# Kernel tuning notes

Measured on AMD Instinct MI355X. Metric: run time of the kernel, lower is better.

Reference implementation:

```python
import jax, jax.numpy as jnp
import numpy as np
from jax import lax

NUM_SUPERNODES = 1024
KNN_K = 16
MIN_GRIPPER = 16
MIN_MASK = 8
GRIP_START = 0
GRIP_RADIUS = 0.1
NEG_INF = -jnp.inf


def _take(a, idx):
    return jnp.take_along_axis(a, idx, axis=1)


def _scatter_or(idx, keep, Bf, N):
    # OR `keep` into a fresh [Bf,N] bool mask at positions idx (mirrors torch scatter_)
    b = jnp.arange(Bf)[:, None]
    return jnp.zeros((Bf, N), dtype=bool).at[b, idx].max(keep)


def _cdist(a, b):
    # a [B,M,3], b [B,N,3] -> [B,M,N] euclidean
    d2 = (jnp.sum(a * a, -1)[:, :, None] + jnp.sum(b * b, -1)[:, None, :]
          - 2.0 * jnp.einsum('bmd,bnd->bmn', a, b))
    return jnp.sqrt(jnp.maximum(d2, 0.0))


def _sample_supernodes(xyz, valid, state, mask_id, extra_scores, global_scores):
    Bf, N, _ = xyz.shape
    M = NUM_SUPERNODES
    valid = valid.astype(bool)
    row_has_valid = valid.any(axis=1)
    first_valid = jnp.argmax(valid, axis=1).astype(jnp.int32)  # [Bf]

    # ---- gripper quota: nearest points to gripper xyz (within radius if any) ----
    k_grip = min(MIN_GRIPPER, M)
    gxyz = state[:, GRIP_START:GRIP_START + 3]
    gdist = jnp.linalg.norm(xyz - gxyz[:, None, :], axis=-1)  # [Bf,N]
    in_radius = gdist <= GRIP_RADIUS
    has_radius = (valid & in_radius).any(axis=1, keepdims=True)
    eligible = valid & (in_radius | ~has_radius)
    dist_rank = jnp.where(eligible, gdist, jnp.inf)
    neg_vals, grip_idx = lax.top_k(-dist_rank, k_grip)
    grip_vals = -neg_vals
    grip_keep = jnp.isfinite(grip_vals) & row_has_valid[:, None]
    head_idx = jnp.where(grip_keep, grip_idx, first_valid[:, None])
    head_bucket = jnp.where(grip_keep, 1, -1)
    selected = _scatter_or(grip_idx, grip_keep, Bf, N)

    remaining = M - k_grip
    # ---- mask-instance quota: one point per mask id (dedup via sort) ----
    mask_cand = valid & ~selected
    sentinel = jnp.iinfo(mask_id.dtype).max
    mask_key = jnp.where(mask_cand, mask_id, sentinel)
    sort_idx = jnp.argsort(mask_key, axis=1)
    sorted_valid = _take(mask_cand, sort_idx)
    sorted_mask = _take(mask_id, sort_idx)
    first_for_id = jnp.concatenate(
        [sorted_valid[:, :1],
         sorted_valid[:, 1:] & (sorted_mask[:, 1:] != sorted_mask[:, :-1])], axis=1)
    pos = jnp.arange(N, dtype=jnp.float32)[None, :]
    mask_scores = jnp.where(first_for_id, -pos, NEG_INF)
    mask_vals, mask_pos = lax.top_k(mask_scores, remaining)
    mask_idx = _take(sort_idx, mask_pos)
    mask_keep = jnp.isfinite(mask_vals) & row_has_valid[:, None]
    selected_after_mask = selected | _scatter_or(mask_idx, mask_keep, Bf, N)

    # ---- extra random mask supernodes to guarantee min_mask quota ----
    k_extra = min(MIN_MASK, remaining)
    es = jnp.where(valid & ~selected_after_mask, extra_scores, NEG_INF)
    extra_vals, extra_idx = lax.top_k(es, k_extra)
    extra_keep = jnp.isfinite(extra_vals) & row_has_valid[:, None]
    use_extra = ~mask_keep[:, :k_extra] & extra_keep
    mask_idx = mask_idx.at[:, :k_extra].set(
        jnp.where(use_extra, extra_idx, mask_idx[:, :k_extra]))
    mask_keep = mask_keep.at[:, :k_extra].set(mask_keep[:, :k_extra] | use_extra)

    # ---- global random fill ----
    selected_for_global = selected | _scatter_or(mask_idx, mask_keep, Bf, N)
    gs = jnp.where(valid & ~selected_for_global, global_scores, NEG_INF)
    gvals, gidx = lax.top_k(gs, remaining)
    gkeep = jnp.isfinite(gvals) & row_has_valid[:, None]
    fill_idx = jnp.where(mask_keep, mask_idx,
                         jnp.where(gkeep, gidx, first_valid[:, None]))
    fill_bucket = jnp.where(mask_keep, 2, jnp.where(gkeep, 0, -1))

    out_idx = jnp.concatenate([head_idx, fill_idx], axis=1)
    out_bucket = jnp.concatenate([head_bucket, fill_bucket], axis=1)
    out_valid = _take(valid, out_idx) & row_has_valid[:, None]
    out_bucket = jnp.where(out_valid, out_bucket, -1)
    return out_idx, out_valid, out_bucket


def setup_inputs() -> dict:
    key = jax.random.key(0)
    ks = jax.random.split(key, 6)
    Bf, N, C = 8, 16384, 64
    return {
        'x': jax.random.normal(ks[0], (Bf, N, C), dtype=jnp.float32),
        'xyz': jax.random.normal(ks[1], (Bf, N, 3), dtype=jnp.float32),
        'valid': jnp.ones((Bf, N), dtype=bool),
        'state': jax.random.normal(ks[2], (Bf, 8), dtype=jnp.float32),
        'mask_id': jax.random.randint(ks[3], (Bf, N), 0, 32, dtype=jnp.int32),
        'extra_scores': jax.random.uniform(ks[4], (Bf, N), dtype=jnp.float32),
        'global_scores': jax.random.uniform(ks[5], (Bf, N), dtype=jnp.float32),
    }


def reference(x, xyz, valid, state, mask_id, extra_scores, global_scores):
    Bf, N, C = x.shape
    out_idx, out_valid, out_bucket = _sample_supernodes(
        xyz, valid, state, mask_id, extra_scores, global_scores)
    # gather_points
    supernode_xyz = _take(xyz, out_idx[:, :, None].repeat(3, axis=2))  # [Bf,M,3]
    # build_knn_neighbors: masked cdist + topk smallest
    dist = _cdist(supernode_xyz.astype(jnp.float32), xyz.astype(jnp.float32))
    dist = jnp.where(valid.astype(bool)[:, None, :], dist, jnp.inf)
    neg_vals, neighbor_idx = lax.top_k(-dist, KNN_K)
    neighbor_mask = jnp.isfinite(-neg_vals)  # [Bf,M,K]
    # gather_neighbors
    b = jnp.arange(Bf)[:, None, None]
    neighbor_feats = x[b, neighbor_idx]  # [Bf,M,K,C]
    return (neighbor_feats, supernode_xyz, neighbor_mask,
            out_idx, out_valid, out_bucket)
```

## Files before the change

### kernel.cpp

```cpp
#include <hip/hip_runtime.h>
#include <math.h>

typedef unsigned long long u64;
typedef unsigned int u32;

#define BF 8
#define NPTS 16384
#define HALFPTS 8192
#define M_SN 1024
#define CCH 64
#define KNN 16
#define NTHR1 1024
#define KPER 16
#define TBL 4096
#define CCAP 2048
#define REM 1008

constexpr size_t O0 = 0;
constexpr size_t O1 = 8388608;
constexpr size_t O2 = 8413184;
constexpr size_t O3 = 8544256;
constexpr size_t O4 = 8552448;
constexpr size_t O5 = 8560640;

#define PW_OFF ((size_t)256)
#define PW_BYTES ((size_t)BF * NPTS * 16)
#define WN_BYTES ((size_t)2 * BF * M_SN * KNN * 8)

__device__ __forceinline__ bool is_valid_el(const void* vp, int mode, long long i) {
  if (mode == 1) return ((const unsigned char*)vp)[i] != 0;
  if (mode == 2) return ((const float*)vp)[i] != 0.0f;
  return ((const int*)vp)[i] != 0;
}

__device__ __forceinline__ u32 desc_enc(float f) {
  u32 u = __float_as_uint(f);
  u32 s = (u & 0x80000000u) ? ~u : (u | 0x80000000u);
  return ~s;
}
__device__ __forceinline__ float desc_dec(u32 e) {
  u32 s = ~e;
  u32 u = (s & 0x80000000u) ? (s & 0x7FFFFFFFu) : ~s;
  return __uint_as_float(u);
}
__device__ __forceinline__ bool enc_finite(u32 d) {
  u32 s = ~d;
  u32 u = (s & 0x80000000u) ? (s & 0x7FFFFFFFu) : ~s;
  return (u & 0x7F800000u) != 0x7F800000u;
}

__device__ __forceinline__ u64 wave_min_u64(u64 v) {
#pragma unroll
  for (int d = 32; d >= 1; d >>= 1) {
    u32 lo = __shfl_xor((u32)(v & 0xFFFFFFFFu), d, 64);
    u32 hi = __shfl_xor((u32)(v >> 32), d, 64);
    u64 o = ((u64)hi << 32) | lo;
    if (o < v) v = o;
  }
  return v;
}

__device__ __forceinline__ u64 block_min_u64(u64 v, u64* red16, int t) {
  v = wave_min_u64(v);
  if ((t & 63) == 0) red16[t >> 6] = v;
  __syncthreads();
  if (t < 64) {
    u64 x = red16[t & 15];
    x = wave_min_u64(x);
    if (t == 0) red16[0] = x;
  }
  __syncthreads();
  u64 r = red16[0];
  __syncthreads();
  return r;
}

__device__ __forceinline__ int block_excl_scan(int val, int* scanb, int t, int* tot) {
  int incl = val;
#pragma unroll
  for (int d = 1; d < 64; d <<= 1) {
    int v = __shfl_up(incl, d, 64);
    if ((t & 63) >= d) incl += v;
  }
  if ((t & 63) == 63) scanb[t >> 6] = incl;
  __syncthreads();
  if (t < 64) {
    int ws = (t < 16) ? scanb[t] : 0;
#pragma unroll
    for (int d = 1; d < 16; d <<= 1) {
      int v = __shfl_up(ws, d, 64);
      if ((t & 63) >= d) ws += v;
    }
    if (t < 16) scanb[16 + t] = ws;
  }
  __syncthreads();
  int wv = t >> 6;
  int base = (wv == 0) ? 0 : scanb[16 + wv - 1];
  *tot = scanb[16 + 15];
  int r = base + incl - val;
  __syncthreads();
  return r;
}

__device__ __forceinline__ u64 shfl64_grp(u64 v, int src) {
  u32 lo = (u32)__shfl((int)(u32)(v & 0xFFFFFFFFu), src, 32);
  u32 hi = (u32)__shfl((int)(u32)(v >> 32), src, 32);
  return ((u64)hi << 32) | lo;
}

template<bool ASC, bool SHIFTBIN>
__device__ __forceinline__ void topk_select(const u32* ek, const u32* bk, u32 cmask,
    int Twant, int* table, u64* cand, int* scanb, int* sh, int* outArr, int t) {
  for (int j = t; j < TBL; j += NTHR1) table[j] = 0;
  if (t == 6) sh[6] = 0x7FFFFFFF;
  if (t == 7) sh[7] = 1;
  __syncthreads();
#pragma unroll
  for (int k = 0; k < KPER; k++) {
    if ((cmask >> k) & 1u) {
      int bin = SHIFTBIN ? (int)(ek[k] >> 20) : (int)bk[k];
      atomicAdd(&table[bin], 1);
    }
  }
  __syncthreads();
  int c_[4]; int c4 = 0;
#pragma unroll
  for (int q = 0; q < 4; q++) { c_[q] = table[4 * t + q]; c4 += c_[q]; }
  int htot;
  int cum = block_excl_scan(c4, scanb, t, &htot);
  const int T = min(Twant, htot);
  int e_ = cum;
#pragma unroll
  for (int q = 0; q < 4; q++) {
    int nx = e_ + c_[q];
    if (T > 0 && e_ < T && nx >= T) atomicMin(&sh[6], 4 * t + q);
    table[4 * t + q] = e_;
    e_ = nx;
  }
  __syncthreads();
  if (T <= 0) return;
  const int B = sh[6];
#pragma unroll
  for (int k = 0; k < KPER; k++) {
    if ((cmask >> k) & 1u) {
      int bin = SHIFTBIN ? (int)(ek[k] >> 20) : (int)bk[k];
      if (bin <= B) {
        int pos = atomicAdd(&table[bin], 1);
        if (pos < CCAP)
          cand[pos] = ((u64)ek[k] << 32) | ((u64)(u32)bin << 14) | (u32)(k * NTHR1 + t);
      }
    }
  }
  __syncthreads();
  const int nc = table[B];
  if (nc <= CCAP) {
    for (int c = t; c < nc; c += NTHR1) {
      u64 key = cand[c];
      int bin = (int)((key >> 14) & 0xFFFu);
      int s = bin ? table[bin - 1] : 0;
      int e2 = table[bin];
      int r = s;
      for (int j = s; j < e2; j++) r += (cand[j] < key);
      if (r < T) {
        u32 enc = (u32)(key >> 32);
        int ix = (int)(key & 0x3FFFu);
        bool fin = ASC ? (enc < 0x7F800000u) : enc_finite(enc);
        outArr[r] = fin ? ix : (ix | (int)0x80000000);
      }
    }
  } else {
    if (t == 0) sh[7] = 0;
  }
  __syncthreads();
}

__global__ void detect_valid(const unsigned* __restrict__ w, int nwords, int* __restrict__ flag) {
  int local = 0;
  for (int i = blockIdx.x * blockDim.x + threadIdx.x; i < nwords; i += gridDim.x * blockDim.x) {
    unsigned v = w[i];
    if (v == 0x3F800000u) local = 2;
    else if (v != 0u && v != 1u) local = max(local, 1);
  }
#pragma unroll
  for (int d = 32; d >= 1; d >>= 1) local = max(local, __shfl_xor(local, d, 64));
  if ((threadIdx.x & 63) == 0 && local) atomicMax(flag, local);
}

__global__ __launch_bounds__(1024)
void sample_kernel(const float* __restrict__ xyz, const void* __restrict__ validp,
                   const float* __restrict__ state, const int* __restrict__ mask_id,
                   const float* __restrict__ extra, const float* __restrict__ glob,
                   const int* __restrict__ flagp, float4* __restrict__ pw,
                   float* __restrict__ out) {
  __shared__ u64 red16[16];
  __shared__ int table[TBL];
  __shared__ int scanb[32];
  __shared__ int mpick[REM];
  __shared__ u64 cand[CCAP];
  __shared__ int gsorted[REM];
  __shared__ int head_i[16];
  __shared__ int head_bk[16];
  __shared__ int sh[8];

  const int b = blockIdx.x, t = threadIdx.x;
  const int vmode = flagp[0];
  const float* xyzb = xyz + (size_t)b * NPTS * 3;
  const int* midb = mask_id + (size_t)b * NPTS;
  const float* exb = extra + (size_t)b * NPTS;
  const float* glb = glob + (size_t)b * NPTS;

  if (t < 8) sh[t] = 0;
  if (t == 1) sh[1] = 0x7FFFFFFF;
  if (t < 16) gsorted[t] = -1;
  __syncthreads();

  u32 vbits = 0;
#pragma unroll
  for (int k = 0; k < KPER; k++) {
    int i = k * NTHR1 + t;
    if (is_valid_el(validp, vmode, (long long)b * NPTS + i)) vbits |= 1u << k;
  }
  if (vbits) {
    atomicOr(&sh[0], 1);
    atomicMin(&sh[1], (__ffs(vbits) - 1) * NTHR1 + t);
  }

  float gx = state[b * 8 + 0], gy = state[b * 8 + 1], gz = state[b * 8 + 2];
  float gd[KPER];
  u32 inr = 0;
#pragma unroll
  for (int k = 0; k < KPER; k++) {
    int i = k * NTHR1 + t;
    float px = xyzb[3 * i], py = xyzb[3 * i + 1], pz = xyzb[3 * i + 2];
    float dx = px - gx, dy = py - gy, dz = pz - gz;
    float d = sqrtf((dx * dx + dy * dy) + dz * dz);
    gd[k] = d;
    bool vb = (vbits >> k) & 1u;
    if (vb && d <= 0.1f) inr |= 1u << k;
    if (pw) {
      float sb = __fadd_rn(__fadd_rn(__fmul_rn(px, px), __fmul_rn(py, py)), __fmul_rn(pz, pz));
      pw[(size_t)b * NPTS + i] = make_float4(px, py, pz, vb ? sb : INFINITY);
    }
  }
  if (inr) atomicOr(&sh[2], 1);
  __syncthreads();

  const int rhv = sh[0];
  const int first_valid = rhv ? sh[1] : 0;
  const u32 elig = vbits & (sh[2] ? inr : 0xFFFFu);
  u32 sel = 0;

  {
    u32 ek[KPER];
#pragma unroll
    for (int k = 0; k < KPER; k++) ek[k] = __float_as_uint(gd[k]);
    topk_select<true, true>(ek, nullptr, elig, 16, table, cand, scanb, sh, gsorted, t);
    if (sh[7]) {
      if (t < 16) {
        int g = gsorted[t];
        head_i[t] = (g >= 0) ? g : first_valid;
        head_bk[t] = (g >= 0) ? 1 : -1;
      }
      __syncthreads();
      for (int j = 0; j < 16; j++) {
        if (head_bk[j] == 1) {
          int ix = head_i[j];
          if ((ix & (NTHR1 - 1)) == t) sel |= 1u << (ix >> 10);
        }
      }
    } else {
      for (int it = 0; it < 16; ++it) {
        u64 best = ~0ull;
#pragma unroll
        for (int k = 0; k < KPER; k++) {
          if (((elig >> k) & 1u) && !((sel >> k) & 1u)) {
            u64 key = ((u64)__float_as_uint(gd[k]) << 32) | (u32)(k * NTHR1 + t);
            if (key < best) best = key;
          }
        }
        u64 w = block_min_u64(best, red16, t);
        bool keep = (w >> 32) < 0x7F800000ull;
        int idx = (int)(w & 0xFFFFFFFFu);
        if (t == 0) { head_i[it] = keep ? idx : first_valid; head_bk[it] = keep ? 1 : -1; }
        if (keep && (idx & (NTHR1 - 1)) == t) sel |= 1u << (idx >> 10);
      }
      __syncthreads();
    }
  }

  for (int j = t; j < TBL; j += NTHR1) table[j] = 0x7FFFFFFF;
  __syncthreads();
#pragma unroll
  for (int k = 0; k < KPER; k++) {
    if (((vbits >> k) & 1u) && !((sel >> k) & 1u)) {
      int i = k * NTHR1 + t;
      int id = midb[i];
      if ((u32)id < TBL) atomicMin(&table[id], i);
    }
  }
  __syncthreads();
  int cnt = 0;
#pragma unroll
  for (int q = 0; q < 4; q++) cnt += (table[4 * t + q] != 0x7FFFFFFF);
  int mtot;
  int excl = block_excl_scan(cnt, scanb, t, &mtot);
  {
    int pos = excl;
#pragma unroll
    for (int q = 0; q < 4; q++) {
      int v = table[4 * t + q];
      if (v != 0x7FFFFFFF) { if (pos < REM) mpick[pos] = v; pos++; }
    }
  }
  __syncthreads();
  const int nm = min(mtot, REM);
  for (int j = 0; j < nm; j++) {
    int p = mpick[j];
    if ((p & (NTHR1 - 1)) == t) sel |= 1u << (p >> 10);
  }

  u32 extra_used = 0;
  if (nm < 8 && rhv) {
    u32 extrbits = 0;
    for (int j = 0; j < 8; j++) {
      u64 best = ~0ull;
#pragma unroll
      for (int k = 0; k < KPER; k++) {
        if (((vbits >> k) & 1u) && !((sel >> k) & 1u) && !((extrbits >> k) & 1u)) {
          int i = k * NTHR1 + t;
          u64 key = ((u64)desc_enc(exb[i]) << 32) | (u32)i;
          if (key < best) best = key;
        }
      }
      u64 w = block_min_u64(best, red16, t);
      if (w == ~0ull) break;
      int idx = (int)(w & 0xFFFFFFFFu);
      bool fin = enc_finite((u32)(w >> 32));
      if ((idx & (NTHR1 - 1)) == t) extrbits |= 1u << (idx >> 10);
      if (j >= nm && fin) {
        extra_used |= 1u << j;
        if (t == 0) mpick[j] = idx;
        if ((idx & (NTHR1 - 1)) == t) sel |= 1u << (idx >> 10);
      }
    }
    __syncthreads();
  }

  {
    u32 cbits = vbits & ~sel;
    u32 ek[KPER], bk[KPER];
#pragma unroll
    for (int k = 0; k < KPER; k++) {
      if ((cbits >> k) & 1u) {
        float f = glb[k * NTHR1 + t];
        ek[k] = desc_enc(f);
        float g = fminf(fmaxf(f, 0.0f), 0.99999994f);
        bk[k] = 4095u - (u32)(g * 4096.0f);
      } else { ek[k] = 0xFFFFFFFFu; bk[k] = 4095u; }
    }
    for (int j = t; j < REM; j += NTHR1) gsorted[j] = -1;
    topk_select<false, false>(ek, bk, cbits, REM, table, cand, scanb, sh, gsorted, t);
    if (!sh[7]) {
      u32 gext = 0;
      for (int j = 0; j < REM; j++) {
        u64 best = ~0ull;
#pragma unroll
        for (int k = 0; k < KPER; k++) {
          if (((cbits >> k) & 1u) && !((gext >> k) & 1u)) {
            u64 key = ((u64)ek[k] << 32) | (u32)(k * NTHR1 + t);
            if (key < best) best = key;
          }
        }
        u64 w = block_min_u64(best, red16, t);
        if (w == ~0ull) break;
        int idx = (int)(w & 0xFFFFFFFFu);
        if ((idx & (NTHR1 - 1)) == t) gext |= 1u << (idx >> 10);
        if (t == 0) gsorted[j] = enc_finite((u32)(w >> 32)) ? idx : (idx | (int)0x80000000);
      }
      __syncthreads();
    }
  }

  {
    int slot = t;
    int idx, bucket;
    if (slot < 16) {
      idx = head_i[slot];
      bucket = head_bk[slot];
    } else {
      int jj = slot - 16;
      bool mk = (jj < nm) || (jj < 8 && ((extra_used >> jj) & 1u));
      if (mk) { idx = mpick[jj]; bucket = 2; }
      else {
        int g = gsorted[jj];
        if (rhv && g >= 0) { idx = g; bucket = 0; }
        else { idx = first_valid; bucket = -1; }
      }
    }
    bool ov = rhv && is_valid_el(validp, vmode, (long long)b * NPTS + idx);
    int ob = ov ? bucket : -1;
    size_t o = (size_t)b * M_SN + slot;
    out[O3 + o] = (float)idx;
    out[O4 + o] = ov ? 1.0f : 0.0f;
    out[O5 + o] = (float)ob;
    out[O1 + 3 * o + 0] = xyzb[3 * idx + 0];
    out[O1 + 3 * o + 1] = xyzb[3 * idx + 1];
    out[O1 + 3 * o + 2] = xyzb[3 * idx + 2];
  }
}

#define NTHR2 256
#define CH 1024
#define SPW 2
#define SNB 8
#define SPB 8

__global__ __launch_bounds__(256, 8)
void knn_kernel(const float* __restrict__ x, const float* __restrict__ xyz,
                const void* __restrict__ validp, const int* __restrict__ flagp,
                const float4* __restrict__ pw, u64* __restrict__ wnws,
                float* __restrict__ out) {
  __shared__ __align__(16) float4 st[CH];
  __shared__ u64 wn[SNB * KNN];

  const int b = blockIdx.x >> 7;
  const int grp = blockIdx.x & 127;
  const int half = blockIdx.y;
  const int t = threadIdx.x;
  const int g = t >> 6;
  const int lane = t & 63;
  const int m0 = grp * SNB + g * SPW;
  const float* xyzb = xyz + (size_t)b * NPTS * 3;
  const long long gbase = (long long)b * NPTS;

  float a2x[SPW], a2y[SPW], a2z[SPW];
#pragma unroll
  for (int s = 0; s < SPW; s++) {
    int sidx = (int)out[O3 + (size_t)b * M_SN + m0 + s];
    float ax, ay, az;
    if (pw) { float4 c = pw[gbase + sidx]; ax = c.x; ay = c.y; az = c.z; }
    else { ax = xyzb[3 * sidx]; ay = xyzb[3 * sidx + 1]; az = xyzb[3 * sidx + 2]; }
    a2x[s] = ax + ax; a2y[s] = ay + ay; a2z[s] = az + az;
  }

  float ld[SPW]; int li[SPW]; float kq[SPW];
#pragma unroll
  for (int s = 0; s < SPW; s++) { ld[s] = -INFINITY; li[s] = 0; kq[s] = -INFINITY; }

  const int vmode = pw ? 0 : flagp[0];
  const int cbeg = wnws ? half * HALFPTS : 0;
  const int cend = wnws ? cbeg + HALFPTS : NPTS;

  for (int c0 = cbeg; c0 < cend; c0 += CH) {
    if (pw) {
      const float4* src = pw + gbase + c0;
#pragma unroll
      for (int qq = 0; qq < CH / NTHR2; qq++) st[t + qq * NTHR2] = src[t + qq * NTHR2];
    } else {
      for (int p = t; p < CH; p += NTHR2) {
        float px = xyzb[3 * (c0 + p)], py = xyzb[3 * (c0 + p) + 1], pz = xyzb[3 * (c0 + p) + 2];
        bool v = is_valid_el(validp, vmode, gbase + c0 + p);
        float sb = __fadd_rn(__fadd_rn(__fmul_rn(px, px), __fmul_rn(py, py)), __fmul_rn(pz, pz));
        st[p] = make_float4(px, py, pz, v ? sb : INFINITY);
      }
    }
    __syncthreads();

    int jstart = 0;
    if (c0 == cbeg) {
      float4 v = st[lane];
#pragma unroll
      for (int s = 0; s < SPW; s++) {
        float qv = __builtin_fmaf(a2x[s], v.x, __builtin_fmaf(a2y[s], v.y, __builtin_fmaf(a2z[s], v.z, -v.w)));
        u64 ku = ((u64)desc_enc(qv) << 32) | (u32)(c0 + lane);
#pragma unroll
        for (int kk = 2; kk <= 64; kk <<= 1) {
#pragma unroll
          for (int jj = kk >> 1; jj > 0; jj >>= 1) {
            u32 olo = (u32)__shfl_xor((int)(u32)(ku & 0xFFFFFFFFu), jj, 64);
            u32 ohi = (u32)__shfl_xor((int)(u32)(ku >> 32), jj, 64);
            u64 o = ((u64)ohi << 32) | olo;
            bool keepmin = ((lane & jj) == 0) == ((lane & kk) == 0);
            ku = ((ku < o) == keepmin) ? ku : o;
          }
        }
        ld[s] = desc_dec((u32)(ku >> 32));
        li[s] = (int)(u32)(ku & 0xFFFFFFFFu);
        kq[s] = __shfl(ld[s], 15, 64);
      }
      jstart = 1;
    }

#pragma unroll 2
    for (int j = jstart; j < CH / 64; j++) {
      float4 v = st[lane + 64 * j];
#pragma unroll
      for (int s = 0; s < SPW; s++) {
        float qv = __builtin_fmaf(a2x[s], v.x, __builtin_fmaf(a2y[s], v.y, __builtin_fmaf(a2z[s], v.z, -v.w)));
        u64 bal = __ballot(qv > kq[s]);
        if (bal) {
          do {
            int bb = __ffsll(bal) - 1;
            bal &= bal - 1;
            float kd = __shfl(qv, bb, 64);
            int ki = c0 + 64 * j + bb;
            bool gt = ld[s] < kd;
            float sd = __shfl_up(ld[s], 1, 64);
            int si = __shfl_up(li[s], 1, 64);
            int pg = __shfl_up(gt ? 1 : 0, 1, 64);
            if (lane == 0) pg = 0;
            ld[s] = gt ? (pg ? sd : kd) : ld[s];
            li[s] = gt ? (pg ? si : ki) : li[s];
          } while (bal);
          kq[s] = __shfl(ld[s], 15, 64);
        }
      }
    }
    __syncthreads();
  }

  if (wnws) {
#pragma unroll
    for (int s = 0; s < SPW; s++)
      if (lane < KNN)
        wnws[((size_t)half * BF + b) * M_SN * KNN + (size_t)(m0 + s) * KNN + lane] =
            ((u64)desc_enc(ld[s]) << 32) | (u32)li[s];
    return;
  }

#pragma unroll
  for (int s = 0; s < SPW; s++)
    if (lane < KNN) wn[(g * SPW + s) * KNN + lane] = ((u64)desc_enc(ld[s]) << 32) | (u32)li[s];
  __syncthreads();
  for (int r = t; r < SNB * KNN; r += NTHR2) {
    u64 key = wn[r];
    int ni = (int)(key & (u64)(NPTS - 1));
    int mm = grp * SNB + (r >> 4);
    size_t o2 = ((size_t)b * M_SN + mm) * KNN + (r & 15);
    out[O2 + o2] = enc_finite((u32)(key >> 32)) ? 1.0f : 0.0f;
    const float4* src = (const float4*)(x + (gbase + ni) * CCH);
    float4* dst = (float4*)(out + O0 + o2 * CCH);
#pragma unroll
    for (int q = 0; q < 16; q++) dst[q] = src[q];
  }
}

__global__ __launch_bounds__(256)
void knn_merge_kernel(const float* __restrict__ x, const u64* __restrict__ wnws,
                      float* __restrict__ out) {
  __shared__ u64 wn[SPB * KNN];
  const int b = blockIdx.x >> 7;
  const int grp = blockIdx.x & 127;
  const int t = threadIdx.x;
  const int sl = t >> 5;
  const int sub = t & 31;
  const int m = grp * SPB + sl;

  const int h = sub >> 4, k = sub & 15;
  u64 my = wnws[((size_t)h * BF + b) * M_SN * KNN + (size_t)m * KNN + k];
  const int obase = (1 - h) << 4;
  int cnt2 = 0;
#pragma unroll
  for (int j = 0; j < 16; j++) {
    u64 o = shfl64_grp(my, obase + j);
    cnt2 += h ? (o <= my) : (o < my);
  }
  int rank = k + cnt2;
  if (rank < KNN) wn[sl * KNN + rank] = my;
  __syncthreads();

  {
    int s2 = t >> 5;
    int k2 = (t >> 1) & 15;
    int hf = t & 1;
    int mm = grp * SPB + s2;
    u64 key = wn[s2 * KNN + k2];
    int ni = (int)(key & (u64)(NPTS - 1));
    size_t o2 = ((size_t)b * M_SN + mm) * KNN + k2;
    if (hf == 0) out[O2 + o2] = enc_finite((u32)(key >> 32)) ? 1.0f : 0.0f;
    const float4* src = (const float4*)(x + ((size_t)b * NPTS + ni) * CCH);
    float4* dst = (float4*)(out + O0 + o2 * CCH);
#pragma unroll
    for (int q = 0; q < 8; q++) dst[hf * 8 + q] = src[hf * 8 + q];
  }
}

extern "C" void kernel_launch(void* const* d_in, const int* in_sizes, int n_in,
                              void* d_out, int out_size, void* d_ws, size_t ws_size,
                              hipStream_t stream) {
  const float* x = (const float*)d_in[0];
  const float* xyz = (const float*)d_in[1];
  const void* valid = d_in[2];
  const float* state = (const float*)d_in[3];
  const int* mask_id = (const int*)d_in[4];
  const float* extra = (const float*)d_in[5];
  const float* glob = (const float*)d_in[6];
  float* out = (float*)d_out;
  int* flag = (int*)d_ws;

  float4* pw = nullptr;
  u64* wnws = nullptr;
  if (ws_size >= PW_OFF + PW_BYTES) pw = (float4*)((char*)d_ws + PW_OFF);
  if (pw && ws_size >= PW_OFF + PW_BYTES + WN_BYTES)
    wnws = (u64*)((char*)d_ws + PW_OFF + PW_BYTES);

  hipMemsetAsync(flag, 0, 4, stream);
  detect_valid<<<64, 1024, 0, stream>>>((const unsigned*)valid, in_sizes[2] / 4, flag);
  sample_kernel<<<BF, NTHR1, 0, stream>>>(xyz, valid, state, mask_id, extra, glob, flag, pw, out);
  dim3 kg(BF * 128, wnws ? 2 : 1);
  knn_kernel<<<kg, NTHR2, 0, stream>>>(x, xyz, valid, flag, pw, wnws, out);
  if (wnws) knn_merge_kernel<<<BF * 128, NTHR2, 0, stream>>>(x, wnws, out);
}
```

Before: 253.1 us.

## Split KNN point range into four segments and fold validity detection into sampler

```diff
diff --git a/kernel.cpp b/kernel.cpp
--- a/kernel.cpp
+++ b/kernel.cpp
@@ -6,7 +6,6 @@
 
 #define BF 8
 #define NPTS 16384
-#define HALFPTS 8192
 #define M_SN 1024
 #define CCH 64
 #define KNN 16
@@ -25,7 +24,7 @@
 
 #define PW_OFF ((size_t)256)
 #define PW_BYTES ((size_t)BF * NPTS * 16)
-#define WN_BYTES ((size_t)2 * BF * M_SN * KNN * 8)
+#define SEG1_BYTES ((size_t)BF * M_SN * KNN * 8)
 
 __device__ __forceinline__ bool is_valid_el(const void* vp, int mode, long long i) {
   if (mode == 1) return ((const unsigned char*)vp)[i] != 0;
@@ -190,8 +189,7 @@
 void sample_kernel(const float* __restrict__ xyz, const void* __restrict__ validp,
                    const float* __restrict__ state, const int* __restrict__ mask_id,
                    const float* __restrict__ extra, const float* __restrict__ glob,
-                   const int* __restrict__ flagp, float4* __restrict__ pw,
-                   float* __restrict__ out) {
+                   int vwords, float4* __restrict__ pw, float* __restrict__ out) {
   __shared__ u64 red16[16];
   __shared__ int table[TBL];
   __shared__ int scanb[32];
@@ -203,7 +201,6 @@
   __shared__ int sh[8];
 
   const int b = blockIdx.x, t = threadIdx.x;
-  const int vmode = flagp[0];
   const float* xyzb = xyz + (size_t)b * NPTS * 3;
   const int* midb = mask_id + (size_t)b * NPTS;
   const float* exb = extra + (size_t)b * NPTS;
@@ -213,6 +210,19 @@
   if (t == 1) sh[1] = 0x7FFFFFFF;
   if (t < 16) gsorted[t] = -1;
   __syncthreads();
+
+  {
+    const unsigned* w = (const unsigned*)validp;
+    int local = 0;
+    for (int i = t; i < vwords; i += NTHR1) {
+      unsigned vv = w[i];
+      if (vv == 0x3F800000u) local = 2;
+      else if (vv != 0u && vv != 1u) local = max(local, 1);
+    }
+    if (local) atomicMax(&sh[3], local);
+  }
+  __syncthreads();
+  const int vmode = sh[3];
 
   u32 vbits = 0;
 #pragma unroll
@@ -411,25 +421,24 @@
 
 #define NTHR2 256
 #define CH 1024
-#define SPW 2
-#define SNB 8
-#define SPB 8
+#define SPW 4
+#define SNB 16
 
 __global__ __launch_bounds__(256, 8)
 void knn_kernel(const float* __restrict__ x, const float* __restrict__ xyz,
                 const void* __restrict__ validp, const int* __restrict__ flagp,
-                const float4* __restrict__ pw, u64* __restrict__ wnws,
+                const float4* __restrict__ pw, u64* __restrict__ wnws, int nseg,
                 float* __restrict__ out) {
   __shared__ __align__(16) float4 st[CH];
   __shared__ u64 wn[SNB * KNN];
 
-  const int b = blockIdx.x >> 7;
-  const int grp = blockIdx.x & 127;
-  const int half = blockIdx.y;
+  const int b = blockIdx.x >> 6;
+  const int snblk = blockIdx.x & 63;
+  const int seg = blockIdx.y;
   const int t = threadIdx.x;
   const int g = t >> 6;
   const int lane = t & 63;
-  const int m0 = grp * SNB + g * SPW;
+  const int m0 = snblk * SNB + g * SPW;
   const float* xyzb = xyz + (size_t)b * NPTS * 3;
   const long long gbase = (long long)b * NPTS;
 
@@ -448,8 +457,9 @@
   for (int s = 0; s < SPW; s++) { ld[s] = -INFINITY; li[s] = 0; kq[s] = -INFINITY; }
 
   const int vmode = pw ? 0 : flagp[0];
-  const int cbeg = wnws ? half * HALFPTS : 0;
-  const int cend = wnws ? cbeg + HALFPTS : NPTS;
+  const int S = NPTS / nseg;
+  const int cbeg = seg * S;
+  const int cend = cbeg + S;
 
   for (int c0 = cbeg; c0 < cend; c0 += CH) {
     if (pw) {
@@ -523,7 +533,7 @@
 #pragma unroll
     for (int s = 0; s < SPW; s++)
       if (lane < KNN)
-        wnws[((size_t)half * BF + b) * M_SN * KNN + (size_t)(m0 + s) * KNN + lane] =
+        wnws[(((size_t)seg * BF + b) * M_SN + (m0 + s)) * KNN + lane] =
             ((u64)desc_enc(ld[s]) << 32) | (u32)li[s];
     return;
   }
@@ -535,7 +545,7 @@
   for (int r = t; r < SNB * KNN; r += NTHR2) {
     u64 key = wn[r];
     int ni = (int)(key & (u64)(NPTS - 1));
-    int mm = grp * SNB + (r >> 4);
+    int mm = snblk * SNB + (r >> 4);
     size_t o2 = ((size_t)b * M_SN + mm) * KNN + (r & 15);
     out[O2 + o2] = enc_finite((u32)(key >> 32)) ? 1.0f : 0.0f;
     const float4* src = (const float4*)(x + (gbase + ni) * CCH);
@@ -545,43 +555,40 @@
   }
 }
 
+#define MSPB 4
 __global__ __launch_bounds__(256)
 void knn_merge_kernel(const float* __restrict__ x, const u64* __restrict__ wnws,
-                      float* __restrict__ out) {
-  __shared__ u64 wn[SPB * KNN];
-  const int b = blockIdx.x >> 7;
-  const int grp = blockIdx.x & 127;
+                      int nseg, float* __restrict__ out) {
+  __shared__ u64 keys[MSPB][64];
+  __shared__ u64 wsel[MSPB][KNN];
+  const int b = blockIdx.x >> 8;
+  const int sn0 = (blockIdx.x & 255) * MSPB;
   const int t = threadIdx.x;
-  const int sl = t >> 5;
-  const int sub = t & 31;
-  const int m = grp * SPB + sl;
-
-  const int h = sub >> 4, k = sub & 15;
-  u64 my = wnws[((size_t)h * BF + b) * M_SN * KNN + (size_t)m * KNN + k];
-  const int obase = (1 - h) << 4;
-  int cnt2 = 0;
-#pragma unroll
-  for (int j = 0; j < 16; j++) {
-    u64 o = shfl64_grp(my, obase + j);
-    cnt2 += h ? (o <= my) : (o < my);
-  }
-  int rank = k + cnt2;
-  if (rank < KNN) wn[sl * KNN + rank] = my;
-  __syncthreads();
-
+  const int s = t >> 6, e = t & 63;
+  const int E = nseg * KNN;
+  if (e < E) {
+    int seg = e >> 4, k = e & 15;
+    keys[s][e] = wnws[(((size_t)seg * BF + b) * M_SN + sn0 + s) * KNN + k];
+  }
+  __syncthreads();
+  if (e < E) {
+    u64 my = keys[s][e];
+    int rk = 0;
+    for (int j = 0; j < E; j++) rk += (keys[s][j] < my);
+    if (rk < KNN) wsel[s][rk] = my;
+  }
+  __syncthreads();
   {
-    int s2 = t >> 5;
-    int k2 = (t >> 1) & 15;
-    int hf = t & 1;
-    int mm = grp * SPB + s2;
-    u64 key = wn[s2 * KNN + k2];
+    int row = t >> 2, q4 = t & 3;
+    u64 key = wsel[row >> 4][row & 15];
     int ni = (int)(key & (u64)(NPTS - 1));
-    size_t o2 = ((size_t)b * M_SN + mm) * KNN + k2;
-    if (hf == 0) out[O2 + o2] = enc_finite((u32)(key >> 32)) ? 1.0f : 0.0f;
+    int mm = sn0 + (row >> 4);
+    size_t o2 = ((size_t)b * M_SN + mm) * KNN + (row & 15);
+    if (q4 == 0) out[O2 + o2] = enc_finite((u32)(key >> 32)) ? 1.0f : 0.0f;
     const float4* src = (const float4*)(x + ((size_t)b * NPTS + ni) * CCH);
     float4* dst = (float4*)(out + O0 + o2 * CCH);
 #pragma unroll
-    for (int q = 0; q < 8; q++) dst[hf * 8 + q] = src[hf * 8 + q];
+    for (int q = 0; q < 4; q++) dst[q4 * 4 + q] = src[q4 * 4 + q];
   }
 }
 
@@ -597,17 +604,25 @@
   const float* glob = (const float*)d_in[6];
   float* out = (float*)d_out;
   int* flag = (int*)d_ws;
+  const int vwords = in_sizes[2] / 4;
 
   float4* pw = nullptr;
   u64* wnws = nullptr;
+  int nseg = 1;
   if (ws_size >= PW_OFF + PW_BYTES) pw = (float4*)((char*)d_ws + PW_OFF);
-  if (pw && ws_size >= PW_OFF + PW_BYTES + WN_BYTES)
-    wnws = (u64*)((char*)d_ws + PW_OFF + PW_BYTES);
-
-  hipMemsetAsync(flag, 0, 4, stream);
-  detect_valid<<<64, 1024, 0, stream>>>((const unsigned*)valid, in_sizes[2] / 4, flag);
-  sample_kernel<<<BF, NTHR1, 0, stream>>>(xyz, valid, state, mask_id, extra, glob, flag, pw, out);
-  dim3 kg(BF * 128, wnws ? 2 : 1);
-  knn_kernel<<<kg, NTHR2, 0, stream>>>(x, xyz, valid, flag, pw, wnws, out);
-  if (wnws) knn_merge_kernel<<<BF * 128, NTHR2, 0, stream>>>(x, wnws, out);
-}
+  if (pw && ws_size >= PW_OFF + PW_BYTES + 4 * SEG1_BYTES) {
+    nseg = 4; wnws = (u64*)((char*)d_ws + PW_OFF + PW_BYTES);
+  } else if (pw && ws_size >= PW_OFF + PW_BYTES + 2 * SEG1_BYTES) {
+    nseg = 2; wnws = (u64*)((char*)d_ws + PW_OFF + PW_BYTES);
+  }
+
+  if (!pw) {
+    hipMemsetAsync(flag, 0, 4, stream);
+    detect_valid<<<64, 1024, 0, stream>>>((const unsigned*)valid, vwords, flag);
+  }
+  sample_kernel<<<BF, NTHR1, 0, stream>>>(xyz, valid, state, mask_id, extra, glob,
+                                          vwords, pw, out);
+  dim3 kg(BF * 64, nseg);
+  knn_kernel<<<kg, NTHR2, 0, stream>>>(x, xyz, valid, flag, pw, wnws, nseg, out);
+  if (nseg > 1) knn_merge_kernel<<<BF * 256, NTHR2, 0, stream>>>(x, wnws, nseg, out);
+}
```

Result: slower. 309.0 us (+22.1%).
